# Kernel tuning notes

Measured on AMD Instinct MI355X. Metric: run time of the kernel, lower is better.

Reference implementation:

```python
import jax, jax.numpy as jnp
import numpy as np

EPS = 1e-8            # torch cosine_similarity eps
RECENCY_WEIGHT = 0.3  # retrieve() default
NOVELTY_SCALE = 10.0  # _compute_novelty divides min dist by 10

B, N, D, K = 32, 1_000_000, 128, 16


def setup_inputs() -> dict:
    key = jax.random.key(0)
    ks = jax.random.split(key, 6)
    query = jax.random.normal(ks[0], (B, D), dtype=jnp.float32)
    memory = jax.random.normal(ks[1], (N, D), dtype=jnp.float32)
    importance = jax.random.uniform(ks[2], (N,), dtype=jnp.float32)
    timestamps = jnp.sort(jax.random.randint(ks[3], (N,), 0, N).astype(jnp.int32))
    Wq = jax.random.normal(ks[4], (D, D), dtype=jnp.float32) / jnp.sqrt(jnp.float32(D))
    bq = jax.random.normal(ks[5], (D,), dtype=jnp.float32) * 0.01
    return {
        "query": query,
        "memory": memory,
        "importance": importance,
        "timestamps": timestamps,
        "Wq": Wq,
        "bq": bq,
        "current_time": N,
        "k": K,
    }


def reference(query, memory, importance, timestamps, Wq, bq, current_time, k):
    # query_net: Linear(item_dim, item_dim)
    q = query @ Wq.T + bq                              # [B, D]

    # --- batched cosine similarity against the whole bank (replaces Python loop) ---
    q_norm = jnp.sqrt(jnp.sum(q * q, axis=-1, keepdims=True))          # [B, 1]
    m_norm = jnp.sqrt(jnp.sum(memory * memory, axis=-1, keepdims=True))  # [N, 1]
    dots = jnp.einsum("bd,nd->bn", q, memory)                          # [B, N]
    sim = dots / jnp.maximum(q_norm * m_norm.T, EPS)                   # [B, N]

    # recency = (timestamp + 1) / (current_time + 1)
    recency = (timestamps.astype(jnp.float32) + 1.0) / (jnp.float32(current_time) + 1.0)  # [N]

    score = (1.0 - RECENCY_WEIGHT) * sim + RECENCY_WEIGHT * recency[None, :]
    score = score * (0.5 + 0.5 * importance)[None, :]                  # [B, N]

    topk_scores, topk_idx = jax.lax.top_k(score, k)                    # [B, k]

    # --- novelty: min L2 distance from q to any stored vector, capped at 1 ---
    # ||q - m||^2 = ||q||^2 + ||m||^2 - 2 q.m
    d2 = q_norm**2 + m_norm.T**2 - 2.0 * dots                          # [B, N]
    min_dist = jnp.sqrt(jnp.maximum(jnp.min(d2, axis=-1), 0.0))        # [B]
    novelty = jnp.minimum(1.0, min_dist / NOVELTY_SCALE)               # [B]

    return topk_scores, topk_idx, novelty
```

## Files before the change

kernel.cpp:

```cpp
#include <hip/hip_runtime.h>
#include <float.h>

#define BQ 32
#define DIM 128
#define TOPK 16
#define G1 768
#define T1 256
#define T2 256
#define NCAND (G1*16)

typedef float f32x16 __attribute__((ext_vector_type(16)));
typedef __bf16 bf16x8 __attribute__((ext_vector_type(8)));
typedef unsigned int u32x4 __attribute__((ext_vector_type(4)));

static __device__ __forceinline__ unsigned cvt_pk_bf16(float a, float b) {
    unsigned r;
    asm("v_cvt_pk_bf16_f32 %0, %1, %2" : "=v"(r) : "v"(a), "v"(b));
    return r;
}

static __device__ __forceinline__ void split3(float f0, float f1,
                                              unsigned &h01, unsigned &m01, unsigned &l01) {
    h01 = cvt_pk_bf16(f0, f1);
    float r0 = f0 - __uint_as_float(h01 << 16);
    float r1 = f1 - __uint_as_float(h01 & 0xffff0000u);
    m01 = cvt_pk_bf16(r0, r1);
    float s0 = r0 - __uint_as_float(m01 << 16);
    float s1 = r1 - __uint_as_float(m01 & 0xffff0000u);
    l01 = cvt_pk_bf16(s0, s1);
}

static __device__ __forceinline__ f32x16 mfma32(u32x4 a, u32x4 b, f32x16 c) {
    return __builtin_amdgcn_mfma_f32_32x32x16_bf16(
        __builtin_bit_cast(bf16x8, a), __builtin_bit_cast(bf16x8, b), c, 0, 0, 0);
}

__global__ void ph0_qproj(const float* __restrict__ query, const float* __restrict__ Wq,
                          const float* __restrict__ bq,
                          float* __restrict__ qT, float* __restrict__ qn2,
                          float* __restrict__ sinvq)
{
    const int b = blockIdx.x;
    const int d = threadIdx.x;
    float s = bq[d];
    #pragma unroll 8
    for (int kk = 0; kk < DIM; ++kk)
        s = fmaf(query[b * DIM + kk], Wq[d * DIM + kk], s);
    qT[d * BQ + b] = s;
    __shared__ float red[DIM];
    red[d] = s * s;
    __syncthreads();
    for (int off = DIM / 2; off >= 1; off >>= 1) {
        if (d < off) red[d] += red[d + off];
        __syncthreads();
    }
    if (d == 0) {
        qn2[b] = red[0];
        sinvq[b] = 1.0f / sqrtf(red[0]);
    }
}

__global__ __launch_bounds__(T1, 3) void ph1_scan(
    const float* __restrict__ mem, const float* __restrict__ imp,
    const int* __restrict__ tsp, const float* __restrict__ qT,
    const float* __restrict__ sinvq, const float* __restrict__ qn2,
    const int* __restrict__ ctp,
    float* __restrict__ cand_sc, int* __restrict__ cand_ix,
    float* __restrict__ minD_ws, int N, int C)
{
    __shared__ float dsc[T1 * TOPK];
    __shared__ int   dix[T1 * TOPK];
    __shared__ float dmn[T1];
    __shared__ float4 cbuf[4][BQ];
    __shared__ float thr_s[BQ];

    const int tid  = threadIdx.x;
    const int wave = tid >> 6;
    const int lane = tid & 63;
    const int qsel = lane & 31;
    const int hsel = lane >> 5;
    const int g = blockIdx.x;
    const int n0 = g * C;
    const int n1 = (n0 + C < N) ? (n0 + C) : N;

    if (tid < BQ) thr_s[tid] = -FLT_MAX;
    __syncthreads();

    const float invct = 1.0f / ((float)(*ctp) + 1.0f);
    const float sq   = sinvq[qsel];
    const float qn2s = qn2[qsel];

    u32x4 Bh[8], Bm[8], Bl[8];
    #pragma unroll
    for (int t = 0; t < 8; ++t) {
        float x[8];
        #pragma unroll
        for (int j = 0; j < 8; ++j)
            x[j] = qT[(t * 16 + hsel * 8 + j) * BQ + qsel];
        #pragma unroll
        for (int p = 0; p < 4; ++p) {
            unsigned h, m, l;
            split3(x[2 * p], x[2 * p + 1], h, m, l);
            Bh[t][p] = h; Bm[t][p] = m; Bl[t][p] = l;
        }
    }

    float top_s[TOPK]; int top_i[TOPK];
    #pragma unroll
    for (int j = 0; j < TOPK; ++j) { top_s[j] = -FLT_MAX; top_i[j] = 0; }
    float mind = FLT_MAX;

    const int rlast = n1 - 1;
    for (int rb = n0 + wave * 32; rb < n1; rb += 4 * 32) {
        const int arow = rb + qsel;
        const int arc  = (arow < rlast) ? arow : rlast;
        const float* rp = mem + (size_t)arc * DIM + hsel * 8;

        f32x16 acc = { 0.f, 0.f, 0.f, 0.f, 0.f, 0.f, 0.f, 0.f,
                       0.f, 0.f, 0.f, 0.f, 0.f, 0.f, 0.f, 0.f };
        float m2p = 0.0f;

        #pragma unroll
        for (int t = 0; t < 8; ++t) {
            const float4 xa = *(const float4*)(rp + t * 16);
            const float4 xb = *(const float4*)(rp + t * 16 + 4);
            const float xs[8] = { xa.x, xa.y, xa.z, xa.w, xb.x, xb.y, xb.z, xb.w };
            u32x4 Ah, Am, Al;
            #pragma unroll
            for (int p = 0; p < 4; ++p) {
                unsigned h, m, l;
                split3(xs[2 * p], xs[2 * p + 1], h, m, l);
                Ah[p] = h; Am[p] = m; Al[p] = l;
                m2p = fmaf(xs[2 * p], xs[2 * p], m2p);
                m2p = fmaf(xs[2 * p + 1], xs[2 * p + 1], m2p);
            }
            acc = mfma32(Al, Bh[t], acc);
            acc = mfma32(Am, Bm[t], acc);
            acc = mfma32(Ah, Bl[t], acc);
            acc = mfma32(Am, Bh[t], acc);
            acc = mfma32(Ah, Bm[t], acc);
            acc = mfma32(Ah, Bh[t], acc);
        }

        const float m2full = m2p + __shfl_xor(m2p, 32);
        const int crow = rb + qsel;
        const int crc  = (crow < rlast) ? crow : rlast;
        const float impf = fmaf(0.5f, imp[crc], 0.5f);
        const float recn = ((float)tsp[crc] + 1.0f) * invct;
        const float invm = rsqrtf(m2full);
        cbuf[wave][qsel] = make_float4(0.7f * invm * impf,
                                       0.3f * recn * impf,
                                       m2full,
                                       (crow < n1) ? 1.0f : -1.0f);
        const float thrq = thr_s[qsel];

        #pragma unroll
        for (int reg = 0; reg < 16; ++reg) {
            const int r = (reg & 3) + 8 * (reg >> 2) + 4 * hsel;
            const float4 cc = cbuf[wave][r];
            const float dot = acc[reg];
            const float score = fmaf(dot, cc.x * sq, cc.y);
            const float d2 = fmaf(-2.0f, dot, qn2s + cc.z);
            if (cc.w > 0.0f) {
                mind = fminf(mind, d2);
                if (score > fmaxf(top_s[TOPK - 1], thrq)) {
                    float cs = score; int ci = rb + r;
                    #pragma unroll
                    for (int p = 0; p < TOPK; ++p) {
                        const bool gt = cs > top_s[p];
                        const float tv = top_s[p]; const int tx = top_i[p];
                        top_s[p] = gt ? cs : tv;  top_i[p] = gt ? ci : tx;
                        cs = gt ? tv : cs;        ci = gt ? tx : ci;
                    }
                }
            }
        }
        if (top_s[TOPK - 1] > thrq) thr_s[qsel] = top_s[TOPK - 1];
    }

    __syncthreads();
    #pragma unroll
    for (int j = 0; j < TOPK; ++j) {
        dsc[tid * TOPK + j] = top_s[j];
        dix[tid * TOPK + j] = top_i[j];
    }
    dmn[tid] = mind;
    __syncthreads();

    for (int qq = 0; qq < 8; ++qq) {
        const int q = wave * 8 + qq;
        float sc2[2]; int ix2[2];
        #pragma unroll
        for (int s = 0; s < 2; ++s) {
            const int c = lane * 2 + s;
            const int L = (c >> 4) * 32 + q;
            const int slot = c & 15;
            sc2[s] = dsc[L * TOPK + slot];
            ix2[s] = dix[L * TOPK + slot];
        }
        float lm = (sc2[0] >= sc2[1]) ? sc2[0] : sc2[1];
        int   ls = (sc2[0] >= sc2[1]) ? 0 : 1;
        for (int r = 0; r < TOPK; ++r) {
            float v = lm; int we = lane;
            #pragma unroll
            for (int off = 32; off >= 1; off >>= 1) {
                const float ov = __shfl_xor(v, off);
                const int   oe = __shfl_xor(we, off);
                if (ov > v || (ov == v && oe < we)) { v = ov; we = oe; }
            }
            if (lane == we) {
                cand_sc[(g * 32 + q) * TOPK + r] = lm;
                cand_ix[(g * 32 + q) * TOPK + r] = ix2[ls];
                sc2[ls] = -FLT_MAX;
                lm = (sc2[0] >= sc2[1]) ? sc2[0] : sc2[1];
                ls = (sc2[0] >= sc2[1]) ? 0 : 1;
            }
        }
    }

    if (tid < 32) {
        float m = FLT_MAX;
        #pragma unroll
        for (int l = 0; l < 8; ++l) m = fminf(m, dmn[l * 32 + tid]);
        minD_ws[g * 32 + tid] = m;
    }
}

__global__ void ph2_final(const float* __restrict__ cand_sc, const int* __restrict__ cand_ix,
                          const float* __restrict__ minD_ws, float* __restrict__ out, int G)
{
    __shared__ float ssc[NCAND];
    __shared__ float shv[4];
    __shared__ int   she[4];
    __shared__ float smin[T2];

    const int q = blockIdx.x;
    const int tid = threadIdx.x;
    const int wave = tid >> 6;
    const int lane = tid & 63;

    for (int e = tid; e < NCAND; e += T2)
        ssc[e] = cand_sc[(e >> 4) * (32 * TOPK) + q * TOPK + (e & 15)];
    __syncthreads();

    float lm = ssc[tid]; int le = tid;
    for (int s = 1; s < NCAND / T2; ++s) {
        const int e = s * T2 + tid;
        const float v = ssc[e];
        if (v > lm) { lm = v; le = e; }
    }

    for (int r = 0; r < TOPK; ++r) {
        float v = lm; int e = le;
        #pragma unroll
        for (int off = 32; off >= 1; off >>= 1) {
            const float ov = __shfl_xor(v, off);
            const int   oe = __shfl_xor(e, off);
            if (ov > v || (ov == v && oe < e)) { v = ov; e = oe; }
        }
        if (lane == 0) { shv[wave] = v; she[wave] = e; }
        __syncthreads();
        float bv = shv[0]; int be = she[0];
        #pragma unroll
        for (int w2 = 1; w2 < 4; ++w2) {
            const float wv = shv[w2]; const int we2 = she[w2];
            if (wv > bv || (wv == bv && we2 < be)) { bv = wv; be = we2; }
        }
        if (le == be) {
            out[q * TOPK + r] = bv;
            const int gix = cand_ix[(be >> 4) * (32 * TOPK) + q * TOPK + (be & 15)];
            out[BQ * TOPK + q * TOPK + r] = (float)gix;
            ssc[le] = -FLT_MAX;
            lm = ssc[tid]; le = tid;
            for (int s = 1; s < NCAND / T2; ++s) {
                const int e2 = s * T2 + tid;
                const float v2 = ssc[e2];
                if (v2 > lm) { lm = v2; le = e2; }
            }
        }
        __syncthreads();
    }

    float m = FLT_MAX;
    for (int g2 = tid; g2 < G; g2 += T2) m = fminf(m, minD_ws[g2 * 32 + q]);
    smin[tid] = m;
    __syncthreads();
    for (int off = T2 / 2; off >= 1; off >>= 1) {
        if (tid < off) smin[tid] = fminf(smin[tid], smin[tid + off]);
        __syncthreads();
    }
    if (tid == 0) {
        const float md = sqrtf(fmaxf(smin[0], 0.0f));
        out[2 * BQ * TOPK + q] = fminf(1.0f, md * 0.1f);
    }
}

extern "C" void kernel_launch(void* const* d_in, const int* in_sizes, int n_in,
                              void* d_out, int out_size, void* d_ws, size_t ws_size,
                              hipStream_t stream) {
    const float* query      = (const float*)d_in[0];
    const float* memory     = (const float*)d_in[1];
    const float* importance = (const float*)d_in[2];
    const int*   timestamps = (const int*)d_in[3];
    const float* Wq         = (const float*)d_in[4];
    const float* bq         = (const float*)d_in[5];
    const int*   ctp        = (const int*)d_in[6];
    const int N = in_sizes[2];

    float* ws      = (float*)d_ws;
    float* qT      = ws;
    float* qn2     = ws + 4096;
    float* sinvq   = ws + 4128;
    float* cand_sc = ws + 4352;
    int*   cand_ix = (int*)(ws + 4352 + G1 * 32 * TOPK);
    float* minD_ws = ws + 4352 + 2 * G1 * 32 * TOPK;

    const int C = (N + G1 - 1) / G1;

    ph0_qproj<<<BQ, DIM, 0, stream>>>(query, Wq, bq, qT, qn2, sinvq);
    ph1_scan<<<G1, T1, 0, stream>>>(memory, importance, timestamps, qT, sinvq, qn2,
                                    ctp, cand_sc, cand_ix, minD_ws, N, C);
    ph2_final<<<BQ, T2, 0, stream>>>(cand_sc, cand_ix, minD_ws, (float*)d_out, G1);
}
```

Before: 866.9 us.

## Software-pipeline memory row loads across iterations in scan kernel

Splits each 32-row tile load into two halves held in register buffers. The first half of the next tile is prefetched while the second half of the current tile is computed, and importance and timestamp loads are issued early. Scheduling barriers keep the loads and the MFMA compute apart so global-memory latency overlaps with the bf16 split-MFMA work. The extra registers force launch bounds down to 2 waves per SIMD, and the grid shrinks from 768 to 512 blocks to match, which trades occupancy for explicit prefetching.

```diff
diff --git a/kernel.cpp b/kernel.cpp
--- a/kernel.cpp
+++ b/kernel.cpp
@@ -4,7 +4,7 @@
 #define BQ 32
 #define DIM 128
 #define TOPK 16
-#define G1 768
+#define G1 512
 #define T1 256
 #define T2 256
 #define NCAND (G1*16)
@@ -34,6 +34,37 @@
     return __builtin_amdgcn_mfma_f32_32x32x16_bf16(
         __builtin_bit_cast(bf16x8, a), __builtin_bit_cast(bf16x8, b), c, 0, 0, 0);
 }
+
+#define LOADH(H, base) \
+    _Pragma("unroll") \
+    for (int j = 0; j < 4; ++j) { \
+        H[2*j]   = *(const float4*)((base) + j*16); \
+        H[2*j+1] = *(const float4*)((base) + j*16 + 4); \
+    }
+
+#define COMPUTEH(H, tb) \
+    _Pragma("unroll") \
+    for (int tt = 0; tt < 4; ++tt) { \
+        const int t = (tb) + tt; \
+        const float4 xa = H[2*tt]; \
+        const float4 xb = H[2*tt+1]; \
+        const float xs[8] = { xa.x, xa.y, xa.z, xa.w, xb.x, xb.y, xb.z, xb.w }; \
+        u32x4 Ah, Am, Al; \
+        _Pragma("unroll") \
+        for (int p = 0; p < 4; ++p) { \
+            unsigned h, m, l; \
+            split3(xs[2*p], xs[2*p+1], h, m, l); \
+            Ah[p] = h; Am[p] = m; Al[p] = l; \
+            m2p = fmaf(xs[2*p], xs[2*p], m2p); \
+            m2p = fmaf(xs[2*p+1], xs[2*p+1], m2p); \
+        } \
+        acc = mfma32(Al, Bh[t], acc); \
+        acc = mfma32(Am, Bm[t], acc); \
+        acc = mfma32(Ah, Bl[t], acc); \
+        acc = mfma32(Am, Bh[t], acc); \
+        acc = mfma32(Ah, Bm[t], acc); \
+        acc = mfma32(Ah, Bh[t], acc); \
+    }
 
 __global__ void ph0_qproj(const float* __restrict__ query, const float* __restrict__ Wq,
                           const float* __restrict__ bq,
@@ -60,7 +91,7 @@
     }
 }
 
-__global__ __launch_bounds__(T1, 3) void ph1_scan(
+__global__ __launch_bounds__(T1, 2) void ph1_scan(
     const float* __restrict__ mem, const float* __restrict__ imp,
     const int* __restrict__ tsp, const float* __restrict__ qT,
     const float* __restrict__ sinvq, const float* __restrict__ qn2,
@@ -111,48 +142,50 @@
     float mind = FLT_MAX;
 
     const int rlast = n1 - 1;
-    for (int rb = n0 + wave * 32; rb < n1; rb += 4 * 32) {
-        const int arow = rb + qsel;
-        const int arc  = (arow < rlast) ? arow : rlast;
-        const float* rp = mem + (size_t)arc * DIM + hsel * 8;
+
+    float4 H0[8], H1[8];
+    int rb = n0 + wave * 32;
+    {
+        const int arow0 = rb + qsel;
+        const int arc0  = (arow0 < rlast) ? arow0 : rlast;
+        const float* rp0 = mem + (size_t)arc0 * DIM + hsel * 8;
+        LOADH(H0, rp0);
+    }
+    const int arowp = rb + qsel;
+    const float* rp = mem + (size_t)((arowp < rlast) ? arowp : rlast) * DIM + hsel * 8;
+
+    for (; rb < n1; rb += 128) {
+        LOADH(H1, rp + 64);
+        const int crow = rb + qsel;
+        const int crc  = (crow < rlast) ? crow : rlast;
+        const float iv = imp[crc];
+        const float tv = (float)tsp[crc];
+        const float thrq = thr_s[qsel];
+        __builtin_amdgcn_sched_barrier(0);
 
         f32x16 acc = { 0.f, 0.f, 0.f, 0.f, 0.f, 0.f, 0.f, 0.f,
                        0.f, 0.f, 0.f, 0.f, 0.f, 0.f, 0.f, 0.f };
         float m2p = 0.0f;
 
-        #pragma unroll
-        for (int t = 0; t < 8; ++t) {
-            const float4 xa = *(const float4*)(rp + t * 16);
-            const float4 xb = *(const float4*)(rp + t * 16 + 4);
-            const float xs[8] = { xa.x, xa.y, xa.z, xa.w, xb.x, xb.y, xb.z, xb.w };
-            u32x4 Ah, Am, Al;
-            #pragma unroll
-            for (int p = 0; p < 4; ++p) {
-                unsigned h, m, l;
-                split3(xs[2 * p], xs[2 * p + 1], h, m, l);
-                Ah[p] = h; Am[p] = m; Al[p] = l;
-                m2p = fmaf(xs[2 * p], xs[2 * p], m2p);
-                m2p = fmaf(xs[2 * p + 1], xs[2 * p + 1], m2p);
-            }
-            acc = mfma32(Al, Bh[t], acc);
-            acc = mfma32(Am, Bm[t], acc);
-            acc = mfma32(Ah, Bl[t], acc);
-            acc = mfma32(Am, Bh[t], acc);
-            acc = mfma32(Ah, Bm[t], acc);
-            acc = mfma32(Ah, Bh[t], acc);
-        }
+        COMPUTEH(H0, 0);
+
+        const int rbn = rb + 128;
+        const int arown = rbn + qsel;
+        const int arcn  = (arown < rlast) ? arown : rlast;
+        const float* rpn = (rbn < n1) ? (mem + (size_t)arcn * DIM + hsel * 8) : rp;
+        LOADH(H0, rpn);
+        __builtin_amdgcn_sched_barrier(0);
+
+        COMPUTEH(H1, 4);
 
         const float m2full = m2p + __shfl_xor(m2p, 32);
-        const int crow = rb + qsel;
-        const int crc  = (crow < rlast) ? crow : rlast;
-        const float impf = fmaf(0.5f, imp[crc], 0.5f);
-        const float recn = ((float)tsp[crc] + 1.0f) * invct;
+        const float impf = fmaf(0.5f, iv, 0.5f);
+        const float recn = (tv + 1.0f) * invct;
         const float invm = rsqrtf(m2full);
         cbuf[wave][qsel] = make_float4(0.7f * invm * impf,
                                        0.3f * recn * impf,
                                        m2full,
                                        (crow < n1) ? 1.0f : -1.0f);
-        const float thrq = thr_s[qsel];
 
         #pragma unroll
         for (int reg = 0; reg < 16; ++reg) {
@@ -168,14 +201,16 @@
                     #pragma unroll
                     for (int p = 0; p < TOPK; ++p) {
                         const bool gt = cs > top_s[p];
-                        const float tv = top_s[p]; const int tx = top_i[p];
-                        top_s[p] = gt ? cs : tv;  top_i[p] = gt ? ci : tx;
-                        cs = gt ? tv : cs;        ci = gt ? tx : ci;
+                        const float tv2 = top_s[p]; const int tx = top_i[p];
+                        top_s[p] = gt ? cs : tv2;  top_i[p] = gt ? ci : tx;
+                        cs = gt ? tv2 : cs;        ci = gt ? tx : ci;
                     }
                 }
             }
         }
         if (top_s[TOPK - 1] > thrq) thr_s[qsel] = top_s[TOPK - 1];
+
+        rp = rpn;
     }
 
     __syncthreads();
```

After: 821.1 us. 1.06x faster.
